# Kernel tuning notes

Measured on AMD Instinct MI355X. Metric: run time of the kernel, lower is better.

The kernel has to match this reference:

```python
import jax, jax.numpy as jnp
import numpy as np

TOP_K = 2
NUM_EXPERTS = 64
SEQ, BS, HS = 2048, 4, 4096
TOKENS = SEQ * BS  # tokens_per_batch
TOL = 1e-4
EPS = 1e-8


def sinkhorn(temp_cost):
    # temp_cost: (T, E) float32 logits. Mirrors SinkhornRouter.sinkhorn exactly.
    cost = jnp.exp(temp_cost)
    n0, n1 = cost.shape
    # initial d0 (overwritten inside loop in torch too, kept for fidelity of carry dtype/shape)
    d0 = (TOKENS / NUM_EXPERTS) * jnp.sum(jnp.exp(2.0 * temp_cost), axis=1)
    d1 = jnp.ones((n1,), dtype=cost.dtype)
    err0 = jnp.asarray(1e9, dtype=cost.dtype)

    def cond(carry):
        _, _, err = carry
        return err > TOL

    def body(carry):
        d0, d1, _ = carry  # d1 here plays the role of d1_old
        d0_new = (1.0 / n0) / (jnp.sum(d1 * cost, axis=1) + EPS)          # (T,)
        d1_new = (1.0 / n1) / (jnp.sum(d0_new[:, None] * cost, axis=0) + EPS)  # (E,)
        err = jnp.mean(jnp.abs(d1 - d1_new))
        return (d0_new, d1_new, err)

    d0, d1, _ = jax.lax.while_loop(cond, body, (d0, d1, err0))
    return d1 * cost * d0[:, None]


def setup_inputs() -> dict:
    key = jax.random.key(0)
    kx, kw = jax.random.split(key)
    x = jax.random.normal(kx, (SEQ, BS, HS), dtype=jnp.float32)
    W = jax.random.normal(kw, (NUM_EXPERTS, HS), dtype=jnp.float32) * 0.02
    return {"x": x, "W": W}


def reference(x, W):
    # router logits: (T, E)
    logits = jnp.reshape(x, (-1, x.shape[-1])) @ W.T
    # Sinkhorn normalization is done in fp32 under no_grad in torch -> stop_gradient
    norm_logits = sinkhorn(jax.lax.stop_gradient(logits).astype(jnp.float32))
    _, indices = jax.lax.top_k(norm_logits, TOP_K)  # (T, top_k) int32
    # top_k > 1 -> softmax activation (fp32, cast back)
    probs = jax.nn.softmax(logits.astype(jnp.float32), axis=-1).astype(logits.dtype)
    scores = jnp.take_along_axis(probs, indices, axis=1)  # (T, top_k)
    return scores, indices
```

## Files before the change

kernel.cpp:

```cpp
#include <hip/hip_runtime.h>
#include <hip/hip_cooperative_groups.h>
#include <math.h>

namespace cg = cooperative_groups;

namespace {
constexpr int kTokens = 8192;
constexpr int kHS = 4096;
constexpr float kTol = 1e-4f;
constexpr float kEps = 1e-8f;
constexpr int kMaxIters = 1000;
constexpr int kSinkBlocks = 64;
constexpr int kSplit = 4;
constexpr size_t kTagFloats = 128;
constexpr size_t kGdataFloats = 2 * 64 * 64;
constexpr size_t kPartOff = kTagFloats + kGdataFloats;
constexpr size_t kPartFloats = (size_t)kTokens * kSplit * 64;
constexpr size_t kWhiOff = kPartOff + kPartFloats;
constexpr size_t kWFragFloats = (size_t)(kHS / 32) * 4 * 64 * 4;
constexpr size_t kWloOff = kWhiOff + kWFragFloats;
constexpr size_t kWsNeedFloats = kWloOff + kWFragFloats;
constexpr size_t kWtpFloats = (size_t)(kHS / 4) * 64 * 4;
}

__device__ __forceinline__ float wave_sum(float v) {
#pragma unroll
  for (int o = 32; o; o >>= 1) v += __shfl_xor(v, o, 64);
  return v;
}

typedef __attribute__((ext_vector_type(8))) short bf16x8;
typedef __attribute__((ext_vector_type(4))) float f32x4;

__device__ __forceinline__ unsigned short f2bf(float x) {
  unsigned u = __builtin_bit_cast(unsigned, x);
  u += 0x7fffu + ((u >> 16) & 1u);
  return (unsigned short)(u >> 16);
}

__device__ __forceinline__ void split8r(const float4 a, const float4 b,
                                        bf16x8& hi, bf16x8& lo) {
  const float v[8] = {a.x, a.y, a.z, a.w, b.x, b.y, b.z, b.w};
#pragma unroll
  for (int j = 0; j < 8; ++j) {
    const unsigned short h = f2bf(v[j]);
    const float hf = __builtin_bit_cast(float, (unsigned)h << 16);
    hi[j] = (short)h;
    lo[j] = (short)f2bf(v[j] - hf);
  }
}

__device__ __forceinline__ void split8(const float* p, bf16x8& hi, bf16x8& lo) {
  split8r(*(const float4*)p, *(const float4*)(p + 4), hi, lo);
}

__global__ void __launch_bounds__(256)
k_wsplit(const float* __restrict__ W, bf16x8* __restrict__ whi,
         bf16x8* __restrict__ wlo) {
  const int idx = blockIdx.x * 256 + threadIdx.x;
  const int lane = idx & 63;
  const int n = (idx >> 6) & 3;
  const int kk = idx >> 8;
  const int e = 16 * n + (lane & 15);
  const int k = kk * 32 + ((lane >> 4) << 3);
  bf16x8 hi, lo;
  split8(W + (size_t)e * kHS + k, hi, lo);
  whi[idx] = hi;
  wlo[idx] = lo;
}

__global__ void __launch_bounds__(256, 5)
k_logits(const float* __restrict__ X, const bf16x8* __restrict__ whi,
         const bf16x8* __restrict__ wlo, float* __restrict__ part) {
  const int tid = threadIdx.x;
  const int lane = tid & 63;
  const int wid = tid >> 6;
  const int tile = blockIdx.x >> 2;
  const int sig = blockIdx.x & 3;
  const int t0 = tile * 16;
  const int r = lane & 15;
  const int g = lane >> 4;
  const int kk0 = sig * 32 + wid * 8;

  const float* xp = X + (size_t)(t0 + r) * kHS + kk0 * 32 + g * 8;
  const bf16x8* bh_base = whi + (size_t)kk0 * 4 * 64 + lane;
  const bf16x8* bl_base = wlo + (size_t)kk0 * 4 * 64 + lane;

  f32x4 acc[4];
#pragma unroll
  for (int n = 0; n < 4; ++n) acc[n] = (f32x4){0.f, 0.f, 0.f, 0.f};

  float4 xa[2][2];
  xa[0][0] = *(const float4*)(xp);
  xa[0][1] = *(const float4*)(xp + 4);
  xa[1][0] = *(const float4*)(xp + 32);
  xa[1][1] = *(const float4*)(xp + 36);

#pragma unroll
  for (int ks = 0; ks < 8; ++ks) {
    bf16x8 bh[4], bl[4];
#pragma unroll
    for (int n = 0; n < 4; ++n) {
      bh[n] = bh_base[(ks * 4 + n) * 64];
      bl[n] = bl_base[(ks * 4 + n) * 64];
    }
    const int cur = ks & 1;
    const float4 x0 = xa[cur][0];
    const float4 x1 = xa[cur][1];
    if (ks + 2 < 8) {
      xa[cur][0] = *(const float4*)(xp + (size_t)(ks + 2) * 32);
      xa[cur][1] = *(const float4*)(xp + (size_t)(ks + 2) * 32 + 4);
    }
    bf16x8 ah, al;
    split8r(x0, x1, ah, al);
#pragma unroll
    for (int n = 0; n < 4; ++n) {
      acc[n] = __builtin_amdgcn_mfma_f32_16x16x32_bf16(ah, bh[n], acc[n],
                                                       0, 0, 0);
      acc[n] = __builtin_amdgcn_mfma_f32_16x16x32_bf16(al, bh[n], acc[n],
                                                       0, 0, 0);
      acc[n] = __builtin_amdgcn_mfma_f32_16x16x32_bf16(ah, bl[n], acc[n],
                                                       0, 0, 0);
    }
  }

  __shared__ __align__(16) float red[4][16][68];
#pragma unroll
  for (int n = 0; n < 4; ++n)
#pragma unroll
    for (int q = 0; q < 4; ++q)
      red[wid][g * 4 + q][n * 16 + r] = acc[n][q];
  __syncthreads();

  const int t = tid >> 4;
  const int e4 = (tid & 15) * 4;
  float4 s = *(const float4*)&red[0][t][e4];
#pragma unroll
  for (int w = 1; w < 4; ++w) {
    const float4 p = *(const float4*)&red[w][t][e4];
    s.x += p.x; s.y += p.y; s.z += p.z; s.w += p.w;
  }
  *(float4*)(part + ((size_t)(tile * 4 + sig) * 16 + t) * 64 + e4) = s;
}

__global__ void __launch_bounds__(1024, 1)
k_sinkhorn(const float* __restrict__ part, float* __restrict__ out,
           unsigned* __restrict__ tags, float* __restrict__ gdata) {
  const int tid = threadIdx.x;
  const int lane = tid & 63;
  const int wid = __builtin_amdgcn_readfirstlane(tid >> 6);
  const int blk = blockIdx.x;
  __shared__ float lds[1024];

  const int t0 = blk * 128 + wid * 8;
  float lg[8], cst[8];
#pragma unroll
  for (int t = 0; t < 8; ++t) {
    const int row = t0 + t;
    const float* pb =
        part + ((size_t)(row >> 4) * kSplit * 16 + (row & 15)) * 64 + lane;
    const float a = pb[0] + pb[1024] + pb[2048] + pb[3072];
    lg[t] = a;
    cst[t] = expf(a);
  }

  float d1 = 1.0f;
  float d0v[8];
  int buf = 0;
  for (int it = 0; it < kMaxIters; ++it) {
    float p = 0.0f;
#pragma unroll
    for (int t = 0; t < 8; ++t) {
      const float s = wave_sum(d1 * cst[t]);
      const float d0t = (1.0f / 8192.0f) / (s + kEps);
      d0v[t] = d0t;
      p = fmaf(d0t, cst[t], p);
    }
    __syncthreads();
    lds[wid * 64 + lane] = p;
    __syncthreads();
    const unsigned want = (unsigned)(it + 1);
    if (wid == 0) {
      float bp = 0.0f;
#pragma unroll
      for (int w = 0; w < 16; ++w) bp += lds[w * 64 + lane];
      __hip_atomic_store(&gdata[((size_t)buf * 64 + blk) * 64 + lane], bp,
                         __ATOMIC_RELAXED, __HIP_MEMORY_SCOPE_AGENT);
      __threadfence();
      if (lane == 0)
        __hip_atomic_store(&tags[buf * 64 + blk], want, __ATOMIC_RELEASE,
                           __HIP_MEMORY_SCOPE_AGENT);
      while (__hip_atomic_load(&tags[buf * 64 + lane], __ATOMIC_ACQUIRE,
                               __HIP_MEMORY_SCOPE_AGENT) != want) {
        __builtin_amdgcn_s_sleep(1);
      }
    }
    __syncthreads();
    float s2 = 0.0f;
#pragma unroll
    for (int i = 0; i < 4; ++i)
      s2 += __hip_atomic_load(
          &gdata[((size_t)buf * 64 + wid * 4 + i) * 64 + lane],
          __ATOMIC_RELAXED, __HIP_MEMORY_SCOPE_AGENT);
    lds[wid * 64 + lane] = s2;
    __syncthreads();
    float colsum = 0.0f;
#pragma unroll
    for (int w = 0; w < 16; ++w) colsum += lds[w * 64 + lane];
    const float d1n = (1.0f / 64.0f) / (colsum + kEps);
    const float err = wave_sum(fabsf(d1 - d1n)) * (1.0f / 64.0f);
    d1 = d1n;
    buf ^= 1;
    if (err <= kTol) break;
  }

#pragma unroll
  for (int t = 0; t < 8; ++t) {
    const float lgv = lg[t];
    float m = lgv;
#pragma unroll
    for (int o = 32; o; o >>= 1) m = fmaxf(m, __shfl_xor(m, o, 64));
    const float ex = expf(lgv - m);
    const float den = wave_sum(ex);
    const float prob = ex / den;

    const float v = (d1 * cst[t]) * d0v[t];
    float v1 = v;
    int i1 = lane;
#pragma unroll
    for (int o = 32; o; o >>= 1) {
      const float ov = __shfl_xor(v1, o, 64);
      const int oi = __shfl_xor(i1, o, 64);
      if (ov > v1 || (ov == v1 && oi < i1)) { v1 = ov; i1 = oi; }
    }
    float v2 = (lane == i1) ? -INFINITY : v;
    int i2 = lane;
#pragma unroll
    for (int o = 32; o; o >>= 1) {
      const float ov = __shfl_xor(v2, o, 64);
      const int oi = __shfl_xor(i2, o, 64);
      if (ov > v2 || (ov == v2 && oi < i2)) { v2 = ov; i2 = oi; }
    }
    const float p1 = __shfl(prob, i1, 64);
    const float p2 = __shfl(prob, i2, 64);
    if (lane == 0) {
      const int row = t0 + t;
      out[row * 2 + 0] = p1;
      out[row * 2 + 1] = p2;
      out[2 * kTokens + row * 2 + 0] = (float)i1;
      out[2 * kTokens + row * 2 + 1] = (float)i2;
    }
  }
}

__global__ void __launch_bounds__(256, 1)
sinkhorn_router(const float* __restrict__ X, const float* __restrict__ W,
                float* __restrict__ out, float* __restrict__ ws) {
  cg::grid_group grid = cg::this_grid();
  const int tid = threadIdx.x;
  const int lane = tid & 63;
  const int wid = __builtin_amdgcn_readfirstlane(tid >> 6);
  const int blk = blockIdx.x;

  float4* wtp = reinterpret_cast<float4*>(ws);
  float* gpart = ws + kWtpFloats;
  __shared__ float lds[256];

  {
    const int j = blk * 256 + tid;
    const int e = j & 63;
    const int k4 = j >> 6;
    wtp[j] = *reinterpret_cast<const float4*>(W + (size_t)e * kHS + 4 * (size_t)k4);
  }
  grid.sync();

  const int t0 = blk * 32 + wid * 8;
  const float* xb = X + (size_t)t0 * kHS;
  float lg[8];
#pragma unroll
  for (int t = 0; t < 8; ++t) lg[t] = 0.0f;

#pragma unroll 2
  for (int k4 = 0; k4 < kHS / 4; ++k4) {
    const float4 w = wtp[k4 * 64 + lane];
#pragma unroll
    for (int t = 0; t < 8; ++t) {
      const float* xr = xb + (size_t)t * kHS + 4 * (size_t)k4;
      float a = lg[t];
      a = fmaf(xr[0], w.x, a);
      a = fmaf(xr[1], w.y, a);
      a = fmaf(xr[2], w.z, a);
      a = fmaf(xr[3], w.w, a);
      lg[t] = a;
    }
  }

  float cst[8];
#pragma unroll
  for (int t = 0; t < 8; ++t) cst[t] = expf(lg[t]);

  float d1 = 1.0f;
  float d0v[8];
  int buf = 0;
  for (int it = 0; it < kMaxIters; ++it) {
    float p = 0.0f;
#pragma unroll
    for (int t = 0; t < 8; ++t) {
      const float s = wave_sum(d1 * cst[t]);
      const float d0t = (1.0f / 8192.0f) / (s + kEps);
      d0v[t] = d0t;
      p = fmaf(d0t, cst[t], p);
    }
    __syncthreads();
    lds[wid * 64 + lane] = p;
    __syncthreads();
    if (wid == 0) {
      const float bp =
          lds[lane] + lds[64 + lane] + lds[128 + lane] + lds[192 + lane];
      gpart[buf * (256 * 64) + blk * 64 + lane] = bp;
    }
    grid.sync();
    const float* gp = gpart + buf * (256 * 64);
    float s = 0.0f;
#pragma unroll 8
    for (int b = 0; b < 64; ++b) s += gp[(wid * 64 + b) * 64 + lane];
    lds[wid * 64 + lane] = s;
    __syncthreads();
    const float colsum =
        lds[lane] + lds[64 + lane] + lds[128 + lane] + lds[192 + lane];
    const float d1n = (1.0f / 64.0f) / (colsum + kEps);
    const float err = wave_sum(fabsf(d1 - d1n)) * (1.0f / 64.0f);
    d1 = d1n;
    buf ^= 1;
    if (err <= kTol) break;
  }

#pragma unroll
  for (int t = 0; t < 8; ++t) {
    const float lgv = lg[t];
    float m = lgv;
#pragma unroll
    for (int o = 32; o; o >>= 1) m = fmaxf(m, __shfl_xor(m, o, 64));
    const float ex = expf(lgv - m);
    const float den = wave_sum(ex);
    const float prob = ex / den;

    const float v = (d1 * cst[t]) * d0v[t];
    float v1 = v;
    int i1 = lane;
#pragma unroll
    for (int o = 32; o; o >>= 1) {
      const float ov = __shfl_xor(v1, o, 64);
      const int oi = __shfl_xor(i1, o, 64);
      if (ov > v1 || (ov == v1 && oi < i1)) { v1 = ov; i1 = oi; }
    }
    float v2 = (lane == i1) ? -INFINITY : v;
    int i2 = lane;
#pragma unroll
    for (int o = 32; o; o >>= 1) {
      const float ov = __shfl_xor(v2, o, 64);
      const int oi = __shfl_xor(i2, o, 64);
      if (ov > v2 || (ov == v2 && oi < i2)) { v2 = ov; i2 = oi; }
    }
    const float p1 = __shfl(prob, i1, 64);
    const float p2 = __shfl(prob, i2, 64);
    if (lane == 0) {
      const int row = t0 + t;
      out[row * 2 + 0] = p1;
      out[row * 2 + 1] = p2;
      out[2 * kTokens + row * 2 + 0] = (float)i1;
      out[2 * kTokens + row * 2 + 1] = (float)i2;
    }
  }
}

extern "C" void kernel_launch(void* const* d_in, const int* in_sizes, int n_in,
                              void* d_out, int out_size, void* d_ws,
                              size_t ws_size, hipStream_t stream) {
  const float* X = (const float*)d_in[0];
  const float* W = (const float*)d_in[1];
  float* out = (float*)d_out;
  float* ws = (float*)d_ws;

  const size_t need = kWsNeedFloats * sizeof(float);
  if (ws_size < need) {
    void* args[] = {(void*)&X, (void*)&W, (void*)&out, (void*)&ws};
    hipLaunchCooperativeKernel((const void*)sinkhorn_router, dim3(256),
                               dim3(256), args, 0, stream);
    return;
  }

  unsigned* tags = reinterpret_cast<unsigned*>(ws);
  float* gdata = ws + kTagFloats;
  float* part = ws + kPartOff;
  bf16x8* whi = reinterpret_cast<bf16x8*>(ws + kWhiOff);
  bf16x8* wlo = reinterpret_cast<bf16x8*>(ws + kWloOff);

  hipLaunchKernelGGL(k_wsplit, dim3((kHS / 32) * 4 * 64 / 256), dim3(256), 0,
                     stream, W, whi, wlo);
  hipLaunchKernelGGL(k_logits, dim3((kTokens / 16) * kSplit), dim3(256), 0,
                     stream, X, whi, wlo, part);
  hipLaunchKernelGGL(k_sinkhorn, dim3(kSinkBlocks), dim3(1024), 0, stream,
                     part, out, tags, gdata);
}
```

Measured before the change: 261.0 us.

## Retile logits GEMM, halve sinkhorn blocks, use tagged 64-bit values for grid sync

The logits kernel now has each block compute 32 tokens over half of K, with double-buffered register loads of W and X, so W fragments are reused across two M tiles and fewer partial sums are written. The sinkhorn kernel runs on 32 blocks of 16 tokens per wave, which cuts the number of participants in each per-iteration grid exchange. The separate tag array plus fence is replaced by 64-bit stores that pack the iteration number with the float partial, so readers poll the data itself, and a memset clears the buffer each call. Costs are higher register pressure (occupancy hint lowered to 2), fewer logits blocks, and more serial work per sinkhorn wave.

```diff
diff --git a/kernel.cpp b/kernel.cpp
--- a/kernel.cpp
+++ b/kernel.cpp
@@ -10,11 +10,10 @@
 constexpr float kTol = 1e-4f;
 constexpr float kEps = 1e-8f;
 constexpr int kMaxIters = 1000;
-constexpr int kSinkBlocks = 64;
-constexpr int kSplit = 4;
-constexpr size_t kTagFloats = 128;
-constexpr size_t kGdataFloats = 2 * 64 * 64;
-constexpr size_t kPartOff = kTagFloats + kGdataFloats;
+constexpr int kSinkBlocks = 32;
+constexpr int kSplit = 2;
+constexpr size_t kGdataFloats = 2 * 64 * 64 * 2;
+constexpr size_t kPartOff = kGdataFloats;
 constexpr size_t kPartFloats = (size_t)kTokens * kSplit * 64;
 constexpr size_t kWhiOff = kPartOff + kPartFloats;
 constexpr size_t kWFragFloats = (size_t)(kHS / 32) * 4 * 64 * 4;
@@ -69,108 +68,140 @@
   wlo[idx] = lo;
 }
 
-__global__ void __launch_bounds__(256, 5)
+__device__ __forceinline__ void ldB(const bf16x8* __restrict__ bhp,
+                                    const bf16x8* __restrict__ blp, int ks,
+                                    bf16x8 (&bh)[4], bf16x8 (&bl)[4]) {
+#pragma unroll
+  for (int n = 0; n < 4; ++n) {
+    bh[n] = bhp[(ks * 4 + n) * 64];
+    bl[n] = blp[(ks * 4 + n) * 64];
+  }
+}
+
+__device__ __forceinline__ void ldX(const float* __restrict__ xp, int ks,
+                                    float4 (&x)[2][2]) {
+#pragma unroll
+  for (int m = 0; m < 2; ++m) {
+    x[m][0] = *(const float4*)(xp + (size_t)(16 * m) * kHS + ks * 32);
+    x[m][1] = *(const float4*)(xp + (size_t)(16 * m) * kHS + ks * 32 + 4);
+  }
+}
+
+__device__ __forceinline__ void mstep(const float4 (&x)[2][2],
+                                      const bf16x8 (&bh)[4],
+                                      const bf16x8 (&bl)[4],
+                                      f32x4 (&acc)[2][4]) {
+#pragma unroll
+  for (int m = 0; m < 2; ++m) {
+    bf16x8 ah, al;
+    split8r(x[m][0], x[m][1], ah, al);
+#pragma unroll
+    for (int n = 0; n < 4; ++n) {
+      acc[m][n] =
+          __builtin_amdgcn_mfma_f32_16x16x32_bf16(ah, bh[n], acc[m][n], 0, 0, 0);
+      acc[m][n] =
+          __builtin_amdgcn_mfma_f32_16x16x32_bf16(al, bh[n], acc[m][n], 0, 0, 0);
+      acc[m][n] =
+          __builtin_amdgcn_mfma_f32_16x16x32_bf16(ah, bl[n], acc[m][n], 0, 0, 0);
+    }
+  }
+}
+
+__global__ void __launch_bounds__(256, 2)
 k_logits(const float* __restrict__ X, const bf16x8* __restrict__ whi,
          const bf16x8* __restrict__ wlo, float* __restrict__ part) {
   const int tid = threadIdx.x;
   const int lane = tid & 63;
   const int wid = tid >> 6;
-  const int tile = blockIdx.x >> 2;
-  const int sig = blockIdx.x & 3;
-  const int t0 = tile * 16;
+  const int tile = blockIdx.x >> 1;
+  const int sig = blockIdx.x & 1;
+  const int t0 = tile * 32;
   const int r = lane & 15;
   const int g = lane >> 4;
-  const int kk0 = sig * 32 + wid * 8;
+  const int kk0 = sig * 64 + wid * 16;
 
   const float* xp = X + (size_t)(t0 + r) * kHS + kk0 * 32 + g * 8;
-  const bf16x8* bh_base = whi + (size_t)kk0 * 4 * 64 + lane;
-  const bf16x8* bl_base = wlo + (size_t)kk0 * 4 * 64 + lane;
-
-  f32x4 acc[4];
-#pragma unroll
-  for (int n = 0; n < 4; ++n) acc[n] = (f32x4){0.f, 0.f, 0.f, 0.f};
-
-  float4 xa[2][2];
-  xa[0][0] = *(const float4*)(xp);
-  xa[0][1] = *(const float4*)(xp + 4);
-  xa[1][0] = *(const float4*)(xp + 32);
-  xa[1][1] = *(const float4*)(xp + 36);
-
-#pragma unroll
-  for (int ks = 0; ks < 8; ++ks) {
-    bf16x8 bh[4], bl[4];
-#pragma unroll
-    for (int n = 0; n < 4; ++n) {
-      bh[n] = bh_base[(ks * 4 + n) * 64];
-      bl[n] = bl_base[(ks * 4 + n) * 64];
-    }
-    const int cur = ks & 1;
-    const float4 x0 = xa[cur][0];
-    const float4 x1 = xa[cur][1];
-    if (ks + 2 < 8) {
-      xa[cur][0] = *(const float4*)(xp + (size_t)(ks + 2) * 32);
-      xa[cur][1] = *(const float4*)(xp + (size_t)(ks + 2) * 32 + 4);
-    }
-    bf16x8 ah, al;
-    split8r(x0, x1, ah, al);
-#pragma unroll
-    for (int n = 0; n < 4; ++n) {
-      acc[n] = __builtin_amdgcn_mfma_f32_16x16x32_bf16(ah, bh[n], acc[n],
-                                                       0, 0, 0);
-      acc[n] = __builtin_amdgcn_mfma_f32_16x16x32_bf16(al, bh[n], acc[n],
-                                                       0, 0, 0);
-      acc[n] = __builtin_amdgcn_mfma_f32_16x16x32_bf16(ah, bl[n], acc[n],
-                                                       0, 0, 0);
-    }
-  }
-
-  __shared__ __align__(16) float red[4][16][68];
-#pragma unroll
-  for (int n = 0; n < 4; ++n)
-#pragma unroll
-    for (int q = 0; q < 4; ++q)
-      red[wid][g * 4 + q][n * 16 + r] = acc[n][q];
+  const bf16x8* bhp = whi + (size_t)kk0 * 4 * 64 + lane;
+  const bf16x8* blp = wlo + (size_t)kk0 * 4 * 64 + lane;
+
+  f32x4 acc[2][4];
+#pragma unroll
+  for (int m = 0; m < 2; ++m)
+#pragma unroll
+    for (int n = 0; n < 4; ++n) acc[m][n] = (f32x4){0.f, 0.f, 0.f, 0.f};
+
+  bf16x8 bhA[4], blA[4], bhB[4], blB[4];
+  float4 xA[2][2], xB[2][2];
+  ldB(bhp, blp, 0, bhA, blA);
+  ldX(xp, 0, xA);
+
+#pragma unroll
+  for (int kp = 0; kp < 8; ++kp) {
+    const int ks = 2 * kp;
+    if (ks + 1 < 16) {
+      ldB(bhp, blp, ks + 1, bhB, blB);
+      ldX(xp, ks + 1, xB);
+    }
+    mstep(xA, bhA, blA, acc);
+    if (ks + 2 < 16) {
+      ldB(bhp, blp, ks + 2, bhA, blA);
+      ldX(xp, ks + 2, xA);
+    }
+    mstep(xB, bhB, blB, acc);
+  }
+
+  __shared__ __align__(16) float red[4][32][68];
+#pragma unroll
+  for (int m = 0; m < 2; ++m)
+#pragma unroll
+    for (int n = 0; n < 4; ++n)
+#pragma unroll
+      for (int q = 0; q < 4; ++q)
+        red[wid][m * 16 + g * 4 + q][n * 16 + r] = acc[m][n][q];
   __syncthreads();
 
-  const int t = tid >> 4;
-  const int e4 = (tid & 15) * 4;
-  float4 s = *(const float4*)&red[0][t][e4];
-#pragma unroll
-  for (int w = 1; w < 4; ++w) {
-    const float4 p = *(const float4*)&red[w][t][e4];
-    s.x += p.x; s.y += p.y; s.z += p.z; s.w += p.w;
-  }
-  *(float4*)(part + ((size_t)(tile * 4 + sig) * 16 + t) * 64 + e4) = s;
+#pragma unroll
+  for (int rep = 0; rep < 2; ++rep) {
+    const int idx = rep * 256 + tid;
+    const int t = idx >> 4;
+    const int e4 = (idx & 15) * 4;
+    float4 s = *(const float4*)&red[0][t][e4];
+#pragma unroll
+    for (int w = 1; w < 4; ++w) {
+      const float4 p = *(const float4*)&red[w][t][e4];
+      s.x += p.x; s.y += p.y; s.z += p.z; s.w += p.w;
+    }
+    *(float4*)(part + ((size_t)(tile * 2 + sig) * 32 + t) * 64 + e4) = s;
+  }
 }
 
 __global__ void __launch_bounds__(1024, 1)
 k_sinkhorn(const float* __restrict__ part, float* __restrict__ out,
-           unsigned* __restrict__ tags, float* __restrict__ gdata) {
+           unsigned long long* __restrict__ gdata) {
   const int tid = threadIdx.x;
   const int lane = tid & 63;
   const int wid = __builtin_amdgcn_readfirstlane(tid >> 6);
   const int blk = blockIdx.x;
   __shared__ float lds[1024];
 
-  const int t0 = blk * 128 + wid * 8;
-  float lg[8], cst[8];
-#pragma unroll
-  for (int t = 0; t < 8; ++t) {
+  const int t0 = blk * 256 + wid * 16;
+  float lg[16], cst[16];
+#pragma unroll
+  for (int t = 0; t < 16; ++t) {
     const int row = t0 + t;
     const float* pb =
-        part + ((size_t)(row >> 4) * kSplit * 16 + (row & 15)) * 64 + lane;
-    const float a = pb[0] + pb[1024] + pb[2048] + pb[3072];
+        part + ((size_t)(row >> 5) * 2 * 32 + (row & 31)) * 64 + lane;
+    const float a = pb[0] + pb[2048];
     lg[t] = a;
     cst[t] = expf(a);
   }
 
   float d1 = 1.0f;
-  float d0v[8];
-  int buf = 0;
+  float d0v[16];
   for (int it = 0; it < kMaxIters; ++it) {
     float p = 0.0f;
 #pragma unroll
-    for (int t = 0; t < 8; ++t) {
+    for (int t = 0; t < 16; ++t) {
       const float s = wave_sum(d1 * cst[t]);
       const float d0t = (1.0f / 8192.0f) / (s + kEps);
       d0v[t] = d0t;
@@ -180,28 +211,30 @@
     lds[wid * 64 + lane] = p;
     __syncthreads();
     const unsigned want = (unsigned)(it + 1);
+    const int buf = it & 1;
     if (wid == 0) {
       float bp = 0.0f;
 #pragma unroll
       for (int w = 0; w < 16; ++w) bp += lds[w * 64 + lane];
-      __hip_atomic_store(&gdata[((size_t)buf * 64 + blk) * 64 + lane], bp,
+      const unsigned long long pk =
+          ((unsigned long long)want << 32) |
+          (unsigned long long)__builtin_bit_cast(unsigned, bp);
+      __hip_atomic_store(&gdata[((size_t)buf * 64 + blk) * 64 + lane], pk,
                          __ATOMIC_RELAXED, __HIP_MEMORY_SCOPE_AGENT);
-      __threadfence();
-      if (lane == 0)
-        __hip_atomic_store(&tags[buf * 64 + blk], want, __ATOMIC_RELEASE,
-                           __HIP_MEMORY_SCOPE_AGENT);
-      while (__hip_atomic_load(&tags[buf * 64 + lane], __ATOMIC_ACQUIRE,
-                               __HIP_MEMORY_SCOPE_AGENT) != want) {
+    }
+    __syncthreads();
+    float s2 = 0.0f;
+#pragma unroll
+    for (int i = 0; i < 2; ++i) {
+      const size_t gi = ((size_t)buf * 64 + wid * 2 + i) * 64 + lane;
+      unsigned long long v;
+      while (((v = __hip_atomic_load(&gdata[gi], __ATOMIC_RELAXED,
+                                     __HIP_MEMORY_SCOPE_AGENT)) >>
+              32) != want) {
         __builtin_amdgcn_s_sleep(1);
       }
-    }
-    __syncthreads();
-    float s2 = 0.0f;
-#pragma unroll
-    for (int i = 0; i < 4; ++i)
-      s2 += __hip_atomic_load(
-          &gdata[((size_t)buf * 64 + wid * 4 + i) * 64 + lane],
-          __ATOMIC_RELAXED, __HIP_MEMORY_SCOPE_AGENT);
+      s2 += __builtin_bit_cast(float, (unsigned)(v & 0xffffffffu));
+    }
     lds[wid * 64 + lane] = s2;
     __syncthreads();
     float colsum = 0.0f;
@@ -210,12 +243,11 @@
     const float d1n = (1.0f / 64.0f) / (colsum + kEps);
     const float err = wave_sum(fabsf(d1 - d1n)) * (1.0f / 64.0f);
     d1 = d1n;
-    buf ^= 1;
     if (err <= kTol) break;
   }
 
 #pragma unroll
-  for (int t = 0; t < 8; ++t) {
+  for (int t = 0; t < 16; ++t) {
     const float lgv = lg[t];
     float m = lgv;
 #pragma unroll
@@ -390,16 +422,16 @@
     return;
   }
 
-  unsigned* tags = reinterpret_cast<unsigned*>(ws);
-  float* gdata = ws + kTagFloats;
+  unsigned long long* gdata = reinterpret_cast<unsigned long long*>(ws);
   float* part = ws + kPartOff;
   bf16x8* whi = reinterpret_cast<bf16x8*>(ws + kWhiOff);
   bf16x8* wlo = reinterpret_cast<bf16x8*>(ws + kWloOff);
 
+  hipMemsetAsync(gdata, 0, kGdataFloats * sizeof(float), stream);
   hipLaunchKernelGGL(k_wsplit, dim3((kHS / 32) * 4 * 64 / 256), dim3(256), 0,
                      stream, W, whi, wlo);
-  hipLaunchKernelGGL(k_logits, dim3((kTokens / 16) * kSplit), dim3(256), 0,
+  hipLaunchKernelGGL(k_logits, dim3((kTokens / 32) * kSplit), dim3(256), 0,
                      stream, X, whi, wlo, part);
   hipLaunchKernelGGL(k_sinkhorn, dim3(kSinkBlocks), dim3(1024), 0, stream,
-                     part, out, tags, gdata);
-}
+                     part, out, gdata);
+}
```

Result: faster. 254.9 us (-2.3%).
